# Optimization experiments

Measured on AMD Instinct MI355X. Metric: run time of the kernel, lower is better.

The kernel has to match this reference:

```python
import jax, jax.numpy as jnp
import numpy as np

K = 9          # kernel points along H (morph=0 -> kernel shape (9,1))
PAD = K // 2   # same padding along H
EPS = 1e-5     # batchnorm eps


def setup_inputs() -> dict:
    key = jax.random.key(0)
    ks = jax.random.split(key, 6)
    B, Cin, Cout, H, W = 4, 64, 64, 160, 160
    x = jax.random.normal(ks[0], (B, Cin, H, W), jnp.float32)
    # offset branch conv: 2*K offset channels, kernel (K,1)
    w_off = jax.random.normal(ks[1], (2 * K, Cin, K, 1), jnp.float32) * 0.05
    b_off = jax.random.normal(ks[2], (2 * K,), jnp.float32) * 0.05
    gamma = jnp.ones((2 * K,), jnp.float32)
    beta = jnp.zeros((2 * K,), jnp.float32)
    # deformable conv weights: kernel (K,1), groups=1
    w_def = jax.random.normal(ks[3], (Cout, Cin, K, 1), jnp.float32) * 0.05
    b_def = jax.random.normal(ks[4], (Cout,), jnp.float32) * 0.05
    return {"x": x, "w_off": w_off, "b_off": b_off, "gamma": gamma,
            "beta": beta, "w_def": w_def, "b_def": b_def}


def _convert_offsets(off):
    # morph=0: even channels (x) -> 0; odd channels (y) -> per-kernel-point cumsum
    c = K // 2
    y = off[:, 1::2]                                            # [B,K,H,W]
    top = jnp.flip(jnp.cumsum(jnp.flip(y[:, :c + 1], 1), 1), 1)  # suffix-cumsum to center
    bot = jnp.cumsum(jnp.concatenate([top[:, c:c + 1], y[:, c + 1:]], 1), 1)
    y_new = jnp.concatenate([top[:, :c], bot], 1)
    return jnp.zeros_like(off).at[:, 1::2].set(y_new)


def _deform_conv(x, off, w, b):
    B, C, H, W = x.shape
    dy = off[:, 0::2]                                           # [B,K,H,W]
    dx = off[:, 1::2]
    ky = jnp.arange(K, dtype=x.dtype).reshape(1, K, 1, 1)
    py = jnp.arange(H, dtype=x.dtype).reshape(1, 1, H, 1) - PAD + ky + dy
    px = jnp.arange(W, dtype=x.dtype).reshape(1, 1, 1, W) + dx
    y0 = jnp.floor(py)
    x0 = jnp.floor(px)
    fy = py - y0
    fx = px - x0
    y0i = y0.astype(jnp.int32)
    x0i = x0.astype(jnp.int32)
    xf = x.reshape(B, C, H * W)

    def gather(yc, xc):
        # zero-padded bilinear corner gather -> [B,C,K,H,W]
        valid = ((yc >= 0) & (yc < H) & (xc >= 0) & (xc < W)).astype(x.dtype)
        lin = jnp.clip(yc, 0, H - 1) * W + jnp.clip(xc, 0, W - 1)
        v = jax.vmap(lambda img, idx: img[:, idx])(xf, lin)
        return v * valid[:, None]

    w00 = ((1 - fy) * (1 - fx))[:, None]
    w01 = ((1 - fy) * fx)[:, None]
    w10 = (fy * (1 - fx))[:, None]
    w11 = (fy * fx)[:, None]
    samples = (w00 * gather(y0i, x0i) + w01 * gather(y0i, x0i + 1)
               + w10 * gather(y0i + 1, x0i) + w11 * gather(y0i + 1, x0i + 1))
    # contract kernel points and input channels
    return jnp.einsum('bckhw,ock->bohw', samples, w[:, :, :, 0]) + b[None, :, None, None]


def reference(x, w_off, b_off, gamma, beta, w_def, b_def):
    # offset branch: conv -> batchnorm (training-mode stats) -> tanh -> snake cumsum
    off = jax.lax.conv_general_dilated(
        x, w_off, (1, 1), ((PAD, PAD), (0, 0)),
        dimension_numbers=('NCHW', 'OIHW', 'NCHW')) + b_off[None, :, None, None]
    mu = off.mean((0, 2, 3), keepdims=True)
    var = off.var((0, 2, 3), keepdims=True)
    off = (off - mu) * jax.lax.rsqrt(var + EPS) * gamma[None, :, None, None] + beta[None, :, None, None]
    off = _convert_offsets(jnp.tanh(off))
    return _deform_conv(x, off, w_def, b_def)
```

## Files before the change

### kernel.cpp

```cpp
#include <hip/hip_runtime.h>
#include <hip/hip_fp16.h>
#include <math.h>

#define HW    25600
#define WID   160
#define HEI   160
#define BB    4
#define CIN   64
#define COUT  64
#define NBN   102400
#define TSTR  162
#define ZROW  640
#define NBKT  32

typedef _Float16 f16x8 __attribute__((ext_vector_type(8)));
typedef float    f32x4 __attribute__((ext_vector_type(4)));

union U4 { int i[4]; f16x8 v; };
union HU { unsigned u; __half2 h; };

__device__ __forceinline__ unsigned short f2h(float f) {
    return __half_as_ushort(__float2half(f));
}

__device__ __forceinline__ float ftanh(float x) {
    float e = __builtin_amdgcn_exp2f(x * 2.8853900817779268f);
    return 1.0f - 2.0f * __builtin_amdgcn_rcpf(e + 1.0f);
}

__global__ __launch_bounds__(256) void p0_prep(
        const float* __restrict__ x, const float* __restrict__ w_def,
        const float* __restrict__ w_off,
        unsigned short* __restrict__ xbT, unsigned short* __restrict__ wtA,
        unsigned short* __restrict__ wofA, float* __restrict__ stats) {
    int t = threadIdx.x;
    int blk = blockIdx.x;
    if (blk >= 640) {
        int wb = blk - 640;
#pragma unroll
        for (int u = 0; u < 18; ++u) {
            int idx = t + (wb * 18 + u) * 256;
            int k = idx >> 12;
            int r = idx & 4095;
            int chalf = r >> 11;
            int og = (r >> 9) & 3;
            int L = (r >> 3) & 63;
            int j = idx & 7;
            int o = og * 16 + (L & 15);
            int c = chalf * 32 + (L >> 4) * 8 + j;
            wtA[idx] = f2h(w_def[(o * CIN + c) * 9 + k]);
        }
        if (wb < 4) {
#pragma unroll
            for (int u = 0; u < 9; ++u) {
                int idx = t + (wb * 9 + u) * 256;
                int jj = idx & 7;
                int L  = (idx >> 3) & 63;
                int ch = (idx >> 9) & 1;
                int k  = idx >> 10;
                int j  = L & 15;
                int c  = ch * 32 + (L >> 4) * 8 + jj;
                wofA[idx] = (j < 9) ? f2h(w_off[((2 * j + 1) * CIN + c) * 9 + k])
                                    : (unsigned short)0;
            }
        } else {
            unsigned* z = (unsigned*)(xbT + ZROW * (WID * 64));
#pragma unroll
            for (int u = 0; u < 5; ++u)
                z[((wb - 4) * 5 + u) * 256 + t] = 0;
        }
        if (wb == 0) {
            stats[t] = 0.f; stats[256 + t] = 0.f;
            stats[512 + t] = 0.f; stats[768 + t] = 0.f;
        }
        return;
    }
    __shared__ __align__(16) unsigned short tile[CIN * TSTR];
    int b = blk / HEI, h = blk % HEI;
    const float* xp = x + (b * CIN) * HW + h * WID;
    unsigned* ti = (unsigned*)tile;
#pragma unroll
    for (int u = 0; u < 10; ++u) {
        int e = t + u * 256;
        int c = e / 40, wq = e - c * 40;
        const float4 v = *(const float4*)(xp + c * HW + 4 * wq);
        unsigned p01 = f2h(v.x) | ((unsigned)f2h(v.y) << 16);
        unsigned p23 = f2h(v.z) | ((unsigned)f2h(v.w) << 16);
        ti[81 * c + 2 * wq]     = p01;
        ti[81 * c + 2 * wq + 1] = p23;
    }
    __syncthreads();
    unsigned* dst = (unsigned*)(xbT + (b * HEI + h) * (WID * 64));
#pragma unroll
    for (int u = 0; u < 20; ++u) {
        int e = t + u * 256;
        int w = e >> 5, cp = e & 31;
        unsigned lo = tile[(2 * cp) * TSTR + w];
        unsigned hi = tile[(2 * cp + 1) * TSTR + w];
        dst[e] = lo | (hi << 16);
    }
}

__global__ __launch_bounds__(320, 4) void k1_offconv_mfma(
        const unsigned short* __restrict__ xbT,
        const unsigned short* __restrict__ wofA,
        const float* __restrict__ b_off,
        float* __restrict__ off_odd, float* __restrict__ stats) {
    int t = threadIdx.x;
    int blk = blockIdx.x;
    int xcd = blk & 7;
    int idx = blk >> 3;
    int b   = idx / 40;
    int r2  = idx - b * 40;
    int h   = xcd * 20 + (r2 >> 1);
    int p0  = (r2 & 1) * 80;
    int wave = t >> 6, lane = t & 63;
    int l15 = lane & 15, q = lane >> 4;
    int px  = p0 + wave * 16 + l15;

    f32x4 acc = (f32x4){0.f, 0.f, 0.f, 0.f};
#pragma unroll
    for (int k = 0; k < 9; ++k) {
        int py  = h + k - 4;
        int row = ((unsigned)py < HEI) ? (b * HEI + py) : ZROW;
        const unsigned short* sp = xbT + row * (WID * 64) + px * 64;
        f16x8 a0 = *(const f16x8*)(wofA + ((k * 2 + 0) * 64 + lane) * 8);
        f16x8 a1 = *(const f16x8*)(wofA + ((k * 2 + 1) * 64 + lane) * 8);
        f16x8 b0 = *(const f16x8*)(sp + q * 8);
        f16x8 b1 = *(const f16x8*)(sp + 32 + q * 8);
        acc = __builtin_amdgcn_mfma_f32_16x16x32_f16(a0, b0, acc, 0, 0, 0);
        acc = __builtin_amdgcn_mfma_f32_16x16x32_f16(a1, b1, acc, 0, 0, 0);
    }

    float sS[4] = {0.f, 0.f, 0.f, 0.f}, sQ[4] = {0.f, 0.f, 0.f, 0.f};
#pragma unroll
    for (int r = 0; r < 4; ++r) {
        int j = q * 4 + r;
        if (j < 9) {
            float v = acc[r] + b_off[2 * j + 1];
            off_odd[(b * 9 + j) * HW + h * WID + px] = v;
            sS[r] = v; sQ[r] = v * v;
        }
    }
#pragma unroll
    for (int o = 1; o < 16; o <<= 1) {
#pragma unroll
        for (int r = 0; r < 4; ++r) {
            sS[r] += __shfl_xor(sS[r], o);
            sQ[r] += __shfl_xor(sQ[r], o);
        }
    }
    __shared__ float redS[5][16], redQ[5][16];
    if (l15 == 0) {
#pragma unroll
        for (int r = 0; r < 4; ++r) {
            int j = q * 4 + r;
            if (j < 9) { redS[wave][j] = sS[r]; redQ[wave][j] = sQ[r]; }
        }
    }
    __syncthreads();
    if (t < 18) {
        int j = (t < 9) ? t : t - 9;
        float v = 0.f;
#pragma unroll
        for (int w = 0; w < 5; ++w)
            v += (t < 9) ? redS[w][j] : redQ[w][j];
        atomicAdd(&stats[(blk & (NBKT - 1)) * 32 + t], v);
    }
}

__global__ __launch_bounds__(256, 5) void k4_deform_mfma(
        const unsigned short* __restrict__ xbT,
        const float* __restrict__ off_odd,
        const float* __restrict__ stats,
        const float* __restrict__ gamma,
        const float* __restrict__ beta,
        const unsigned short* __restrict__ wtA,
        const float* __restrict__ b_def,
        float* __restrict__ out) {
    __shared__ __align__(16) int S[2][80 * 36];
    __shared__ unsigned P0h[9][80], P1h[9][80];
    __shared__ int      PXI[9][80];
    __shared__ float    ssum[18];

    int t   = threadIdx.x;
    int blk = blockIdx.x;
    int xcd = blk & 7;
    int idx = blk >> 3;
    int b   = idx / 40;
    int r2  = idx - b * 40;
    int h   = xcd * 20 + (r2 >> 1);
    int p0  = (r2 & 1) * 80;
    int wave = t >> 6, lane = t & 63;
    int l15 = lane & 15, q = lane >> 4;

    if (t < 18) {
        float v = 0.f;
#pragma unroll
        for (int xx = 0; xx < NBKT; ++xx) v += stats[xx * 32 + t];
        ssum[t] = v;
    }
    __syncthreads();

    if (t < 160) {
        int half = (t >= 80) ? 1 : 0;
        int pxl  = t - half * 80;
        int px   = p0 + pxl;
        int j0   = half * 4;
        float tv[5];
#pragma unroll
        for (int u = 0; u < 5; ++u) {
            int j = j0 + u;
            float mean = ssum[j] * (1.0f / NBN);
            float var  = ssum[9 + j] * (1.0f / NBN) - mean * mean;
            float inv  = rsqrtf(var + 1e-5f);
            float v = off_odd[(b * 9 + j) * HW + h * WID + px];
            tv[u] = ftanh((v - mean) * inv * gamma[2 * j + 1] + beta[2 * j + 1]);
        }
        float dxv[5];
        if (half == 0) {
            dxv[4] = tv[4];
#pragma unroll
            for (int i = 3; i >= 0; --i) dxv[i] = dxv[i + 1] + tv[i];
        } else {
            dxv[0] = tv[0];
#pragma unroll
            for (int i = 1; i < 5; ++i) dxv[i] = dxv[i - 1] + tv[i];
        }
#pragma unroll
        for (int u = 0; u < 5; ++u) {
            int j = j0 + u;
            int py = h + j - 4;
            bool rowok = (py >= 0) && (py < HEI);
            float pxf = (float)px + dxv[u];
            float x0f = floorf(pxf);
            float fx  = pxf - x0f;
            int   x0  = (int)x0f;
            float s0f = (rowok && x0 >= 0 && x0 < WID) ? 1.f - fx : 0.f;
            float s1f = (rowok && x0 >= -1 && x0 < WID - 1) ? fx : 0.f;
            unsigned h0 = f2h(s0f), h1 = f2h(s1f);
            P0h[j][pxl] = h0 | (h0 << 16);
            P1h[j][pxl] = h1 | (h1 << 16);
            int xi0 = min(max(x0, 0), WID - 1);
            int xi1 = min(max(x0 + 1, 0), WID - 1);
            PXI[j][pxl] = xi0 | (xi1 << 16);
        }
    }
    __syncthreads();

    f32x4 acc[5];
#pragma unroll
    for (int i = 0; i < 5; ++i) acc[i] = (f32x4){0.f, 0.f, 0.f, 0.f};

    int4     A4[3], B4[3];
    unsigned sa[3], sb[3];
    f16x8    wpa, wpb;

#define PF(kk)                                                                  \
    {                                                                           \
        int pyc = min(max(h + (kk) - 4, 0), HEI - 1);                           \
        const int4* rowI4 = (const int4*)(xbT + (b * HEI + pyc) * (WID * 64));  \
        _Pragma("unroll")                                                       \
        for (int u = 0; u < 3; ++u) {                                           \
            if (u < 2 || t < 128) {                                             \
                int id = t + u * 256;                                           \
                int pxl = id >> 3, c4 = id & 7;                                 \
                int xi = PXI[kk][pxl];                                          \
                sa[u] = P0h[kk][pxl];                                           \
                sb[u] = P1h[kk][pxl];                                           \
                A4[u] = rowI4[(xi & 0xffff) * 8 + c4];                          \
                B4[u] = rowI4[(xi >> 16) * 8 + c4];                             \
            }                                                                   \
        }                                                                       \
        wpa = *(const f16x8*)(wtA + ((((kk) * 2 + 0) * 4 + wave) * 64 + lane) * 8); \
        wpb = *(const f16x8*)(wtA + ((((kk) * 2 + 1) * 4 + wave) * 64 + lane) * 8); \
    }

    PF(0);
    int buf = 0;

    for (int k = 0; k < 9; ++k) {
        int* Sb = S[buf];
#pragma unroll
        for (int u = 0; u < 3; ++u) {
            if (u < 2 || t < 128) {
                int id = t + u * 256;
                int pxl = id >> 3, c4 = id & 7;
                HU sah, sbh; sah.u = sa[u]; sbh.u = sb[u];
                int4 r4;
                HU a, bb, r;
#pragma unroll
                for (int ii = 0; ii < 4; ++ii) {
                    a.u  = (unsigned)(&A4[u].x)[ii];
                    bb.u = (unsigned)(&B4[u].x)[ii];
                    r.h  = __hfma2(sbh.h, bb.h, __hmul2(sah.h, a.h));
                    (&r4.x)[ii] = (int)r.u;
                }
                *(int4*)(Sb + pxl * 36 + (c4 << 2)) = r4;
            }
        }
        __syncthreads();

        f16x8 wf0 = wpa, wf1 = wpb;
        if (k < 8) PF(k + 1);

#pragma unroll
        for (int pxt = 0; pxt < 5; ++pxt) {
            const int* sp = &Sb[(pxt * 16 + l15) * 36];
            U4 u0, u1;
            *(int4*)u0.i = *(const int4*)(sp + q * 4);
            *(int4*)u1.i = *(const int4*)(sp + 16 + q * 4);
            acc[pxt] = __builtin_amdgcn_mfma_f32_16x16x32_f16(wf0, u0.v, acc[pxt], 0, 0, 0);
            acc[pxt] = __builtin_amdgcn_mfma_f32_16x16x32_f16(wf1, u1.v, acc[pxt], 0, 0, 0);
        }
        buf ^= 1;
    }
#undef PF

    float bd[4];
#pragma unroll
    for (int r = 0; r < 4; ++r) bd[r] = b_def[wave * 16 + q * 4 + r];
#pragma unroll
    for (int pxt = 0; pxt < 5; ++pxt) {
#pragma unroll
        for (int r = 0; r < 4; ++r) {
            int o = wave * 16 + q * 4 + r;
            out[(b * COUT + o) * HW + h * WID + p0 + pxt * 16 + l15] = acc[pxt][r] + bd[r];
        }
    }
}

extern "C" void kernel_launch(void* const* d_in, const int* in_sizes, int n_in,
                              void* d_out, int out_size, void* d_ws, size_t ws_size,
                              hipStream_t stream) {
    const float* x     = (const float*)d_in[0];
    const float* w_off = (const float*)d_in[1];
    const float* b_off = (const float*)d_in[2];
    const float* gamma = (const float*)d_in[3];
    const float* beta  = (const float*)d_in[4];
    const float* w_def = (const float*)d_in[5];
    const float* b_def = (const float*)d_in[6];
    float* out = (float*)d_out;

    float* off_odd       = (float*)d_ws;
    float* stats         = off_odd + 921600;
    unsigned short* wtA  = (unsigned short*)(stats + 1024);
    unsigned short* wofA = wtA + 36864;
    unsigned short* xbT  = wofA + 9216;

    p0_prep<<<648, 256, 0, stream>>>(x, w_def, w_off, xbT, wtA, wofA, stats);
    k1_offconv_mfma<<<1280, 320, 0, stream>>>(xbT, wofA, b_off, off_odd, stats);
    k4_deform_mfma<<<1280, 256, 0, stream>>>(xbT, off_odd, stats, gamma, beta,
                                             wtA, b_def, out);
}
```

Before: 127.7 us.

## Build deform MFMA B-operands directly in registers, dropping shared staging buffer

The deform kernel now runs 5 waves of 320 threads, each owning 16 output pixels across all 64 output channels. Each lane gathers and bilinearly blends its own fp16 input values straight into MFMA B-operand registers, so the double-buffered shared-memory sample tile and its per-kernel-point barrier go away. In exchange, weight fragments for all four output-channel groups are reloaded from global memory per kernel point. The software prefetch of the next kernel point's gathers is removed, so load latency is hidden only by occupancy and the partial unroll.

```diff
diff --git a/kernel.cpp b/kernel.cpp
--- a/kernel.cpp
+++ b/kernel.cpp
@@ -169,7 +169,7 @@
     }
 }
 
-__global__ __launch_bounds__(256, 5) void k4_deform_mfma(
+__global__ __launch_bounds__(320, 4) void k4_deform_mfma(
         const unsigned short* __restrict__ xbT,
         const float* __restrict__ off_odd,
         const float* __restrict__ stats,
@@ -178,7 +178,6 @@
         const unsigned short* __restrict__ wtA,
         const float* __restrict__ b_def,
         float* __restrict__ out) {
-    __shared__ __align__(16) int S[2][80 * 36];
     __shared__ unsigned P0h[9][80], P1h[9][80];
     __shared__ int      PXI[9][80];
     __shared__ float    ssum[18];
@@ -193,6 +192,7 @@
     int p0  = (r2 & 1) * 80;
     int wave = t >> 6, lane = t & 63;
     int l15 = lane & 15, q = lane >> 4;
+    int pxl = wave * 16 + l15;
 
     if (t < 18) {
         float v = 0.f;
@@ -204,8 +204,8 @@
 
     if (t < 160) {
         int half = (t >= 80) ? 1 : 0;
-        int pxl  = t - half * 80;
-        int px   = p0 + pxl;
+        int pp   = t - half * 80;
+        int px   = p0 + pp;
         int j0   = half * 4;
         float tv[5];
 #pragma unroll
@@ -239,93 +239,60 @@
             float s0f = (rowok && x0 >= 0 && x0 < WID) ? 1.f - fx : 0.f;
             float s1f = (rowok && x0 >= -1 && x0 < WID - 1) ? fx : 0.f;
             unsigned h0 = f2h(s0f), h1 = f2h(s1f);
-            P0h[j][pxl] = h0 | (h0 << 16);
-            P1h[j][pxl] = h1 | (h1 << 16);
+            P0h[j][pp] = h0 | (h0 << 16);
+            P1h[j][pp] = h1 | (h1 << 16);
             int xi0 = min(max(x0, 0), WID - 1);
             int xi1 = min(max(x0 + 1, 0), WID - 1);
-            PXI[j][pxl] = xi0 | (xi1 << 16);
+            PXI[j][pp] = xi0 | (xi1 << 16);
         }
     }
     __syncthreads();
 
-    f32x4 acc[5];
-#pragma unroll
-    for (int i = 0; i < 5; ++i) acc[i] = (f32x4){0.f, 0.f, 0.f, 0.f};
-
-    int4     A4[3], B4[3];
-    unsigned sa[3], sb[3];
-    f16x8    wpa, wpb;
-
-#define PF(kk)                                                                  \
-    {                                                                           \
-        int pyc = min(max(h + (kk) - 4, 0), HEI - 1);                           \
-        const int4* rowI4 = (const int4*)(xbT + (b * HEI + pyc) * (WID * 64));  \
-        _Pragma("unroll")                                                       \
-        for (int u = 0; u < 3; ++u) {                                           \
-            if (u < 2 || t < 128) {                                             \
-                int id = t + u * 256;                                           \
-                int pxl = id >> 3, c4 = id & 7;                                 \
-                int xi = PXI[kk][pxl];                                          \
-                sa[u] = P0h[kk][pxl];                                           \
-                sb[u] = P1h[kk][pxl];                                           \
-                A4[u] = rowI4[(xi & 0xffff) * 8 + c4];                          \
-                B4[u] = rowI4[(xi >> 16) * 8 + c4];                             \
-            }                                                                   \
-        }                                                                       \
-        wpa = *(const f16x8*)(wtA + ((((kk) * 2 + 0) * 4 + wave) * 64 + lane) * 8); \
-        wpb = *(const f16x8*)(wtA + ((((kk) * 2 + 1) * 4 + wave) * 64 + lane) * 8); \
-    }
-
-    PF(0);
-    int buf = 0;
-
+    f32x4 acc[4];
+#pragma unroll
+    for (int g = 0; g < 4; ++g) acc[g] = (f32x4){0.f, 0.f, 0.f, 0.f};
+
+#pragma unroll 3
     for (int k = 0; k < 9; ++k) {
-        int* Sb = S[buf];
-#pragma unroll
-        for (int u = 0; u < 3; ++u) {
-            if (u < 2 || t < 128) {
-                int id = t + u * 256;
-                int pxl = id >> 3, c4 = id & 7;
-                HU sah, sbh; sah.u = sa[u]; sbh.u = sb[u];
-                int4 r4;
-                HU a, bb, r;
-#pragma unroll
-                for (int ii = 0; ii < 4; ++ii) {
-                    a.u  = (unsigned)(&A4[u].x)[ii];
-                    bb.u = (unsigned)(&B4[u].x)[ii];
-                    r.h  = __hfma2(sbh.h, bb.h, __hmul2(sah.h, a.h));
-                    (&r4.x)[ii] = (int)r.u;
-                }
-                *(int4*)(Sb + pxl * 36 + (c4 << 2)) = r4;
-            }
-        }
-        __syncthreads();
-
-        f16x8 wf0 = wpa, wf1 = wpb;
-        if (k < 8) PF(k + 1);
-
-#pragma unroll
-        for (int pxt = 0; pxt < 5; ++pxt) {
-            const int* sp = &Sb[(pxt * 16 + l15) * 36];
-            U4 u0, u1;
-            *(int4*)u0.i = *(const int4*)(sp + q * 4);
-            *(int4*)u1.i = *(const int4*)(sp + 16 + q * 4);
-            acc[pxt] = __builtin_amdgcn_mfma_f32_16x16x32_f16(wf0, u0.v, acc[pxt], 0, 0, 0);
-            acc[pxt] = __builtin_amdgcn_mfma_f32_16x16x32_f16(wf1, u1.v, acc[pxt], 0, 0, 0);
-        }
-        buf ^= 1;
-    }
-#undef PF
-
-    float bd[4];
-#pragma unroll
-    for (int r = 0; r < 4; ++r) bd[r] = b_def[wave * 16 + q * 4 + r];
-#pragma unroll
-    for (int pxt = 0; pxt < 5; ++pxt) {
+        int pyc = min(max(h + k - 4, 0), HEI - 1);
+        const int4* rowI4 = (const int4*)(xbT + (b * HEI + pyc) * (WID * 64));
+        int xi = PXI[k][pxl];
+        HU s0; s0.u = P0h[k][pxl];
+        HU s1; s1.u = P1h[k][pxl];
+        int i0 = (xi & 0xffff) * 8 + q;
+        int i1 = (xi >> 16) * 8 + q;
+        int4 A0 = rowI4[i0];
+        int4 B0 = rowI4[i1];
+        int4 A1 = rowI4[i0 + 4];
+        int4 B1 = rowI4[i1 + 4];
+        U4 f0, f1;
+#pragma unroll
+        for (int ii = 0; ii < 4; ++ii) {
+            HU a, bb, r;
+            a.u  = (unsigned)(&A0.x)[ii];
+            bb.u = (unsigned)(&B0.x)[ii];
+            r.h  = __hfma2(s1.h, bb.h, __hmul2(s0.h, a.h));
+            f0.i[ii] = (int)r.u;
+            a.u  = (unsigned)(&A1.x)[ii];
+            bb.u = (unsigned)(&B1.x)[ii];
+            r.h  = __hfma2(s1.h, bb.h, __hmul2(s0.h, a.h));
+            f1.i[ii] = (int)r.u;
+        }
+#pragma unroll
+        for (int g = 0; g < 4; ++g) {
+            f16x8 w0 = *(const f16x8*)(wtA + (((k * 2 + 0) * 4 + g) * 64 + lane) * 8);
+            f16x8 w1 = *(const f16x8*)(wtA + (((k * 2 + 1) * 4 + g) * 64 + lane) * 8);
+            acc[g] = __builtin_amdgcn_mfma_f32_16x16x32_f16(w0, f0.v, acc[g], 0, 0, 0);
+            acc[g] = __builtin_amdgcn_mfma_f32_16x16x32_f16(w1, f1.v, acc[g], 0, 0, 0);
+        }
+    }
+
+#pragma unroll
+    for (int g = 0; g < 4; ++g) {
 #pragma unroll
         for (int r = 0; r < 4; ++r) {
-            int o = wave * 16 + q * 4 + r;
-            out[(b * COUT + o) * HW + h * WID + p0 + pxt * 16 + l15] = acc[pxt][r] + bd[r];
+            int o = g * 16 + q * 4 + r;
+            out[(b * COUT + o) * HW + h * WID + p0 + pxl] = acc[g][r] + b_def[o];
         }
     }
 }
@@ -350,6 +317,6 @@
 
     p0_prep<<<648, 256, 0, stream>>>(x, w_def, w_off, xbT, wtA, wofA, stats);
     k1_offconv_mfma<<<1280, 320, 0, stream>>>(xbT, wofA, b_off, off_odd, stats);
-    k4_deform_mfma<<<1280, 256, 0, stream>>>(xbT, off_odd, stats, gamma, beta,
+    k4_deform_mfma<<<1280, 320, 0, stream>>>(xbT, off_odd, stats, gamma, beta,
                                              wtA, b_def, out);
 }
```

After: 149.6 us. +17.1%, slower.

## Repartition deform MFMA work so each of five waves owns a pixel tile

Applied to the files above, without the earlier changes.

The deform kernel moves from 256 to 320 threads, so the sampling phase divides evenly into two gather iterations per thread with no tail guard. Each wave now owns a 16-pixel tile and accumulates all 64 output channels across four MFMA groups, instead of each wave owning 16 output channels over all 80 pixels. Each wave therefore reads one LDS sample fragment per kernel tap and loads weights directly from global memory. This cuts LDS reads but raises weight loads per wave, and it changes register pressure and the occupancy target.

```diff
diff --git a/kernel.cpp b/kernel.cpp
--- a/kernel.cpp
+++ b/kernel.cpp
@@ -169,7 +169,7 @@
     }
 }
 
-__global__ __launch_bounds__(256, 5) void k4_deform_mfma(
+__global__ __launch_bounds__(320, 4) void k4_deform_mfma(
         const unsigned short* __restrict__ xbT,
         const float* __restrict__ off_odd,
         const float* __restrict__ stats,
@@ -204,8 +204,8 @@
 
     if (t < 160) {
         int half = (t >= 80) ? 1 : 0;
-        int pxl  = t - half * 80;
-        int px   = p0 + pxl;
+        int pp   = t - half * 80;
+        int px   = p0 + pp;
         int j0   = half * 4;
         float tv[5];
 #pragma unroll
@@ -239,93 +239,86 @@
             float s0f = (rowok && x0 >= 0 && x0 < WID) ? 1.f - fx : 0.f;
             float s1f = (rowok && x0 >= -1 && x0 < WID - 1) ? fx : 0.f;
             unsigned h0 = f2h(s0f), h1 = f2h(s1f);
-            P0h[j][pxl] = h0 | (h0 << 16);
-            P1h[j][pxl] = h1 | (h1 << 16);
+            P0h[j][pp] = h0 | (h0 << 16);
+            P1h[j][pp] = h1 | (h1 << 16);
             int xi0 = min(max(x0, 0), WID - 1);
             int xi1 = min(max(x0 + 1, 0), WID - 1);
-            PXI[j][pxl] = xi0 | (xi1 << 16);
+            PXI[j][pp] = xi0 | (xi1 << 16);
         }
     }
     __syncthreads();
 
-    f32x4 acc[5];
-#pragma unroll
-    for (int i = 0; i < 5; ++i) acc[i] = (f32x4){0.f, 0.f, 0.f, 0.f};
-
-    int4     A4[3], B4[3];
-    unsigned sa[3], sb[3];
-    f16x8    wpa, wpb;
+    f32x4 acc[4];
+#pragma unroll
+    for (int g = 0; g < 4; ++g) acc[g] = (f32x4){0.f, 0.f, 0.f, 0.f};
+
+    int4     A4[2], B4[2];
+    unsigned sa[2], sb[2];
 
 #define PF(kk)                                                                  \
     {                                                                           \
         int pyc = min(max(h + (kk) - 4, 0), HEI - 1);                           \
         const int4* rowI4 = (const int4*)(xbT + (b * HEI + pyc) * (WID * 64));  \
         _Pragma("unroll")                                                       \
-        for (int u = 0; u < 3; ++u) {                                           \
-            if (u < 2 || t < 128) {                                             \
-                int id = t + u * 256;                                           \
-                int pxl = id >> 3, c4 = id & 7;                                 \
-                int xi = PXI[kk][pxl];                                          \
-                sa[u] = P0h[kk][pxl];                                           \
-                sb[u] = P1h[kk][pxl];                                           \
-                A4[u] = rowI4[(xi & 0xffff) * 8 + c4];                          \
-                B4[u] = rowI4[(xi >> 16) * 8 + c4];                             \
-            }                                                                   \
+        for (int u = 0; u < 2; ++u) {                                           \
+            int id = t + u * 320;                                               \
+            int pxl = id >> 3, c4 = id & 7;                                     \
+            int xi = PXI[kk][pxl];                                              \
+            sa[u] = P0h[kk][pxl];                                               \
+            sb[u] = P1h[kk][pxl];                                               \
+            A4[u] = rowI4[(xi & 0xffff) * 8 + c4];                              \
+            B4[u] = rowI4[(xi >> 16) * 8 + c4];                                 \
         }                                                                       \
-        wpa = *(const f16x8*)(wtA + ((((kk) * 2 + 0) * 4 + wave) * 64 + lane) * 8); \
-        wpb = *(const f16x8*)(wtA + ((((kk) * 2 + 1) * 4 + wave) * 64 + lane) * 8); \
     }
 
     PF(0);
     int buf = 0;
 
+#pragma unroll
     for (int k = 0; k < 9; ++k) {
         int* Sb = S[buf];
 #pragma unroll
-        for (int u = 0; u < 3; ++u) {
-            if (u < 2 || t < 128) {
-                int id = t + u * 256;
-                int pxl = id >> 3, c4 = id & 7;
-                HU sah, sbh; sah.u = sa[u]; sbh.u = sb[u];
-                int4 r4;
-                HU a, bb, r;
-#pragma unroll
-                for (int ii = 0; ii < 4; ++ii) {
-                    a.u  = (unsigned)(&A4[u].x)[ii];
-                    bb.u = (unsigned)(&B4[u].x)[ii];
-                    r.h  = __hfma2(sbh.h, bb.h, __hmul2(sah.h, a.h));
-                    (&r4.x)[ii] = (int)r.u;
-                }
-                *(int4*)(Sb + pxl * 36 + (c4 << 2)) = r4;
+        for (int u = 0; u < 2; ++u) {
+            int id = t + u * 320;
+            int pxl = id >> 3, c4 = id & 7;
+            HU sah, sbh; sah.u = sa[u]; sbh.u = sb[u];
+            int4 r4;
+            HU a, bb, r;
+#pragma unroll
+            for (int ii = 0; ii < 4; ++ii) {
+                a.u  = (unsigned)(&A4[u].x)[ii];
+                bb.u = (unsigned)(&B4[u].x)[ii];
+                r.h  = __hfma2(sbh.h, bb.h, __hmul2(sah.h, a.h));
+                (&r4.x)[ii] = (int)r.u;
             }
+            *(int4*)(Sb + pxl * 36 + (c4 << 2)) = r4;
         }
         __syncthreads();
 
-        f16x8 wf0 = wpa, wf1 = wpb;
         if (k < 8) PF(k + 1);
 
-#pragma unroll
-        for (int pxt = 0; pxt < 5; ++pxt) {
-            const int* sp = &Sb[(pxt * 16 + l15) * 36];
-            U4 u0, u1;
-            *(int4*)u0.i = *(const int4*)(sp + q * 4);
-            *(int4*)u1.i = *(const int4*)(sp + 16 + q * 4);
-            acc[pxt] = __builtin_amdgcn_mfma_f32_16x16x32_f16(wf0, u0.v, acc[pxt], 0, 0, 0);
-            acc[pxt] = __builtin_amdgcn_mfma_f32_16x16x32_f16(wf1, u1.v, acc[pxt], 0, 0, 0);
+        const int* sp = &Sb[(wave * 16 + l15) * 36];
+        U4 u0, u1;
+        *(int4*)u0.i = *(const int4*)(sp + q * 4);
+        *(int4*)u1.i = *(const int4*)(sp + 16 + q * 4);
+#pragma unroll
+        for (int g = 0; g < 4; ++g) {
+            f16x8 w0 = *(const f16x8*)(wtA + (((k * 2 + 0) * 4 + g) * 64 + lane) * 8);
+            f16x8 w1 = *(const f16x8*)(wtA + (((k * 2 + 1) * 4 + g) * 64 + lane) * 8);
+            acc[g] = __builtin_amdgcn_mfma_f32_16x16x32_f16(w0, u0.v, acc[g], 0, 0, 0);
+            acc[g] = __builtin_amdgcn_mfma_f32_16x16x32_f16(w1, u1.v, acc[g], 0, 0, 0);
         }
         buf ^= 1;
     }
 #undef PF
 
-    float bd[4];
-#pragma unroll
-    for (int r = 0; r < 4; ++r) bd[r] = b_def[wave * 16 + q * 4 + r];
-#pragma unroll
-    for (int pxt = 0; pxt < 5; ++pxt) {
+#pragma unroll
+    for (int g = 0; g < 4; ++g) {
 #pragma unroll
         for (int r = 0; r < 4; ++r) {
-            int o = wave * 16 + q * 4 + r;
-            out[(b * COUT + o) * HW + h * WID + p0 + pxt * 16 + l15] = acc[pxt][r] + bd[r];
+            int o = g * 16 + q * 4 + r;
+            out[(b * COUT + o) * HW + h * WID + p0 + wave * 16 + l15] =
+                acc[g][r] + b_def[o];
         }
     }
 }
@@ -350,6 +343,6 @@
 
     p0_prep<<<648, 256, 0, stream>>>(x, w_def, w_off, xbT, wtA, wofA, stats);
     k1_offconv_mfma<<<1280, 320, 0, stream>>>(xbT, wofA, b_off, off_odd, stats);
-    k4_deform_mfma<<<1280, 256, 0, stream>>>(xbT, off_odd, stats, gamma, beta,
+    k4_deform_mfma<<<1280, 320, 0, stream>>>(xbT, off_odd, stats, gamma, beta,
                                              wtA, b_def, out);
 }
```

Result: slower. 140.6 us (+10.1%).
